# Kernel optimization log

Hardware: AMD Instinct MI355X
Metric: run time of the kernel (lower is better)

Reference implementation:

```python
import jax, jax.numpy as jnp
import numpy as np

M_POOL = 5000  # rows of down_transform (coarse mesh size)


def setup_inputs() -> dict:
    key = jax.random.key(0)
    ks = jax.random.split(key, 6)
    bs, n_nodes, c_in, seq_len, c_out = 16, 20000, 32, 9, 64
    x = jax.random.normal(ks[0], (bs, n_nodes, c_in), dtype=jnp.float32)
    indices = jax.random.randint(ks[1], (n_nodes, seq_len), 0, n_nodes, dtype=jnp.int32)
    # xavier-uniform-ish linear weight
    fan_in, fan_out = c_in * seq_len, c_out
    limit = float(np.sqrt(6.0 / (fan_in + fan_out)))
    weight = jax.random.uniform(ks[2], (c_out, fan_in), minval=-limit, maxval=limit, dtype=jnp.float32)
    bias = jnp.zeros((c_out,), dtype=jnp.float32)
    trans_rows = jax.random.randint(ks[3], (20000,), 0, M_POOL, dtype=jnp.int32)
    trans_cols = jax.random.randint(ks[4], (20000,), 0, n_nodes, dtype=jnp.int32)
    trans_vals = jax.random.uniform(ks[5], (20000,), dtype=jnp.float32)
    return {"x": x, "indices": indices, "weight": weight, "bias": bias,
            "trans_rows": trans_rows, "trans_cols": trans_cols, "trans_vals": trans_vals}


def reference(x, indices, weight, bias, trans_rows, trans_cols, trans_vals):
    bs = x.shape[0]
    n_nodes, seq_len = indices.shape
    # SpiralConv: gather spiral neighborhoods -> [bs, n_nodes, seq_len*c_in]
    g = x[:, indices.reshape(-1), :].reshape(bs, n_nodes, -1)
    h = jnp.einsum('bnk,ok->bno', g, weight) + bias  # [bs, n_nodes, c_out]
    h = jax.nn.elu(h)
    # Pool: sparse down_transform @ h  (scatter_add over COO entries)
    contrib = h[:, trans_cols, :] * trans_vals[None, :, None]  # [bs, nnz, c_out]
    out = jnp.zeros((bs, M_POOL, h.shape[-1]), dtype=h.dtype)
    out = out.at[:, trans_rows, :].add(contrib)
    return out
```

## Files before the change

kernel.cpp:

```cpp
#include <hip/hip_runtime.h>

#define BS 16
#define NNODES 20000
#define CIN 32
#define SEQ 9
#define COUT 64
#define KTOT 288
#define MPOOL 5000
#define NNZ 20000

#define H_BYTES   40960000ULL
#define XB_BYTES  20480000ULL
#define WF_BYTES  36864ULL
#define CV_BYTES  (NNZ * 8ULL)
#define START_BYTES ((MPOOL + 1) * 4ULL)
#define CNTCUR_BYTES (2ULL * MPOOL * 4ULL)

#define XBLK (NNODES / 4)
#define WBLK 9
#define ZBLK 10

typedef __attribute__((ext_vector_type(8))) short bf16x8;
typedef __attribute__((ext_vector_type(4))) float f32x4;

static __device__ __forceinline__ unsigned short f2bf(float f) {
  unsigned u = __float_as_uint(f);
  u += 0x7FFF + ((u >> 16) & 1);
  return (unsigned short)(u >> 16);
}
static __device__ __forceinline__ float bf2f(unsigned short s) {
  return __uint_as_float(((unsigned)s) << 16);
}
static __device__ __forceinline__ unsigned cvt_pk_bf16(float lo, float hi) {
  unsigned r;
  asm("v_cvt_pk_bf16_f32 %0, %1, %2" : "=v"(r) : "v"(lo), "v"(hi));
  return r;
}

__global__ __launch_bounds__(256) void prep_kernel(const float* __restrict__ x,
                                                   const float* __restrict__ weight,
                                                   unsigned short* __restrict__ xbT2,
                                                   unsigned short* __restrict__ wf,
                                                   int* __restrict__ cntcur) {
  const int id = blockIdx.x;
  if (id < XBLK) {
    const int W = id * 4 + (threadIdx.x >> 6);
    const int lane = threadIdx.x & 63;
    const unsigned b = (unsigned)W / 1250u;
    const unsigned tile = (unsigned)W % 1250u;
    const int n = (int)tile * 16 + (lane >> 2);
    const int c8 = (lane & 3) * 8;
    const float* src = x + ((size_t)b * NNODES + n) * CIN + c8;
    const float4 u0 = ((const float4*)src)[0];
    const float4 u1 = ((const float4*)src)[1];
    uint4 p;
    p.x = (unsigned)f2bf(u0.x) | ((unsigned)f2bf(u0.y) << 16);
    p.y = (unsigned)f2bf(u0.z) | ((unsigned)f2bf(u0.w) << 16);
    p.z = (unsigned)f2bf(u1.x) | ((unsigned)f2bf(u1.y) << 16);
    p.w = (unsigned)f2bf(u1.z) | ((unsigned)f2bf(u1.w) << 16);
    const int g = (int)(b >> 1), bl = (int)(b & 1);
    *(uint4*)&xbT2[((size_t)g * NNODES + n) * 64 + bl * 32 + c8] = p;
  } else if (id < XBLK + WBLK) {
    const int t = (id - XBLK) * 256 + threadIdx.x;
    if (t < SEQ * 4 * 64) {
      const int f0 = t * 8;
      const int blk = f0 >> 9;
      const int inb = f0 & 511;
      const int lhi = inb >> 7;
      const int l16 = (inb >> 3) & 15;
      const int kk = blk >> 2, o = blk & 3;
      const float* src = weight + (size_t)(o * 16 + l16) * KTOT + kk * 32 + lhi * 8;
      const float4 u0 = ((const float4*)src)[0];
      const float4 u1 = ((const float4*)src)[1];
      uint4 p;
      p.x = (unsigned)f2bf(u0.x) | ((unsigned)f2bf(u0.y) << 16);
      p.y = (unsigned)f2bf(u0.z) | ((unsigned)f2bf(u0.w) << 16);
      p.z = (unsigned)f2bf(u1.x) | ((unsigned)f2bf(u1.y) << 16);
      p.w = (unsigned)f2bf(u1.z) | ((unsigned)f2bf(u1.w) << 16);
      *(uint4*)&wf[f0] = p;
    }
  } else {
    const int base = (id - XBLK - WBLK) * 1024 + threadIdx.x;
#pragma unroll
    for (int j = 0; j < 4; ++j) {
      const int i = base + j * 256;
      if (i < 2 * MPOOL) cntcur[i] = 0;
    }
  }
}

__global__ __launch_bounds__(256) void hist_kernel(const int* __restrict__ rows,
                                                   int* __restrict__ cnt) {
  const int k = blockIdx.x * 256 + threadIdx.x;
  if (k < NNZ) atomicAdd(&cnt[rows[k]], 1);
}

__global__ __launch_bounds__(256) void scan_kernel(const int* __restrict__ cnt,
                                                   int* __restrict__ start) {
  __shared__ int part[256];
  const int t = threadIdx.x;
  const int base = t * 20;
  int local[20];
  int s = 0;
#pragma unroll
  for (int j = 0; j < 20; ++j) {
    const int i = base + j;
    local[j] = s;
    s += (i < MPOOL) ? cnt[i] : 0;
  }
  part[t] = s;
  __syncthreads();
  for (int off = 1; off < 256; off <<= 1) {
    const int v = (t >= off) ? part[t - off] : 0;
    __syncthreads();
    part[t] += v;
    __syncthreads();
  }
  const int excl = (t == 0) ? 0 : part[t - 1];
#pragma unroll
  for (int j = 0; j < 20; ++j) {
    const int i = base + j;
    if (i < MPOOL) start[i] = excl + local[j];
  }
  if (t == 255) start[MPOOL] = NNZ;
}

__global__ __launch_bounds__(256) void reorder_kernel(const int* __restrict__ rows,
                                                      const int* __restrict__ cols,
                                                      const float* __restrict__ vals,
                                                      const int* __restrict__ start,
                                                      int* __restrict__ cursor,
                                                      int2* __restrict__ cvp) {
  const int k = blockIdx.x * 256 + threadIdx.x;
  if (k < NNZ) {
    const int r = rows[k];
    const int pos = start[r] + atomicAdd(&cursor[r], 1);
    cvp[pos] = make_int2(cols[k], __float_as_int(vals[k]));
  }
}

__global__ __launch_bounds__(512, 8) void gemm_elu_kernel(
    const unsigned short* __restrict__ xbT2,
    const int* __restrict__ indices,
    const unsigned short* __restrict__ wf,
    const float* __restrict__ bias,
    unsigned* __restrict__ hT)
{
  __shared__ unsigned short wlds[SEQ * 4 * 512];
  __shared__ int idx_lds[64 * SEQ];

  const int tid = threadIdx.x;
  const int g = blockIdx.x & 7;
  const int n0 = (blockIdx.x >> 3) * 64;

  {
    const uint4* src = (const uint4*)wf;
    uint4* dst = (uint4*)wlds;
    for (int i = tid; i < (SEQ * 4 * 512 * 2) / 16; i += 512)
      dst[i] = src[i];
  }
  for (int i = tid; i < 64 * SEQ; i += 512) {
    const int gidx = n0 * SEQ + i;
    idx_lds[i] = (gidx < NNODES * SEQ) ? indices[gidx] : 0;
  }
  __syncthreads();

  const int wv = tid >> 6;
  const int lane = tid & 63;
  const int l16 = lane & 15;
  const int lhi = lane >> 4;
  const int n0w = n0 + wv * 8;
  if (n0w >= NNODES) return;

  const unsigned short* __restrict__ xg = xbT2 + (size_t)g * NNODES * 64;
  const int moff = (l16 & 1) * 32 + lhi * 8;
  const int boff = lane * 8;
  const int idxbase = (wv * 8 + (l16 >> 1)) * SEQ;

  f32x4 acc[4];
#pragma unroll
  for (int o = 0; o < 4; ++o) {
    f32x4 z = {0.f, 0.f, 0.f, 0.f};
    acc[o] = z;
  }

#pragma unroll
  for (int kk = 0; kk < SEQ; ++kk) {
    const int gi = idx_lds[idxbase + kk];
    const bf16x8 af = *(const bf16x8*)&xg[(size_t)gi * 64 + moff];
    const bf16x8 b0 = *(const bf16x8*)&wlds[(kk * 4 + 0) * 512 + boff];
    const bf16x8 b1 = *(const bf16x8*)&wlds[(kk * 4 + 1) * 512 + boff];
    const bf16x8 b2 = *(const bf16x8*)&wlds[(kk * 4 + 2) * 512 + boff];
    const bf16x8 b3 = *(const bf16x8*)&wlds[(kk * 4 + 3) * 512 + boff];
    acc[0] = __builtin_amdgcn_mfma_f32_16x16x32_bf16(af, b0, acc[0], 0, 0, 0);
    acc[1] = __builtin_amdgcn_mfma_f32_16x16x32_bf16(af, b1, acc[1], 0, 0, 0);
    acc[2] = __builtin_amdgcn_mfma_f32_16x16x32_bf16(af, b2, acc[2], 0, 0, 0);
    acc[3] = __builtin_amdgcn_mfma_f32_16x16x32_bf16(af, b3, acc[3], 0, 0, 0);
  }

  unsigned* __restrict__ hg = hT + (size_t)g * NNODES * 64;
  const int nA = n0w + lhi * 2;
#pragma unroll
  for (int o = 0; o < 4; ++o) {
    const int oc = o * 16 + l16;
    const float bv = bias[oc];
    float v0 = acc[o][0] + bv, v1 = acc[o][1] + bv;
    float v2 = acc[o][2] + bv, v3 = acc[o][3] + bv;
    v0 = v0 > 0.f ? v0 : (__expf(v0) - 1.f);
    v1 = v1 > 0.f ? v1 : (__expf(v1) - 1.f);
    v2 = v2 > 0.f ? v2 : (__expf(v2) - 1.f);
    v3 = v3 > 0.f ? v3 : (__expf(v3) - 1.f);
    hg[(size_t)nA * 64 + oc]       = cvt_pk_bf16(v0, v1);
    hg[(size_t)(nA + 1) * 64 + oc] = cvt_pk_bf16(v2, v3);
  }
}

__global__ __launch_bounds__(256) void pool_kernel(
    const unsigned* __restrict__ hT,
    const int* __restrict__ start,
    const int2* __restrict__ cvp,
    float* __restrict__ out)
{
  const int r = blockIdx.x * 4 + (threadIdx.x >> 6);
  const int lane = threadIdx.x & 63;

  float acc[16];
#pragma unroll
  for (int b = 0; b < 16; ++b) acc[b] = 0.f;

  const int s = start[r], e = start[r + 1];
  int2 cv = (s < e) ? cvp[s] : make_int2(0, 0);
  for (int j = s; j < e; ++j) {
    const int2 cvn = (j + 1 < e) ? cvp[j + 1] : make_int2(0, 0);
    const int c = cv.x;
    const float v = __int_as_float(cv.y);
#pragma unroll
    for (int g = 0; g < 8; ++g) {
      const unsigned u = hT[((size_t)g * NNODES + c) * 64 + lane];
      acc[2 * g]     += v * bf2f((unsigned short)(u & 0xffff));
      acc[2 * g + 1] += v * bf2f((unsigned short)(u >> 16));
    }
    cv = cvn;
  }
#pragma unroll
  for (int b = 0; b < 16; ++b)
    out[((size_t)b * MPOOL + r) * COUT + lane] = acc[b];
}

__global__ __launch_bounds__(256) void scatter_kernel(
    const unsigned* __restrict__ hT,
    const int* __restrict__ rows,
    const int* __restrict__ cols,
    const float* __restrict__ vals,
    float* __restrict__ out)
{
  const int gw = (int)((blockIdx.x * blockDim.x + threadIdx.x) >> 6);
  const int lane = threadIdx.x & 63;
  const int nw = (int)((gridDim.x * blockDim.x) >> 6);
  for (int t = gw; t < NNZ * BS; t += nw) {
    const int k = t >> 4;
    const int b = t & 15;
    const unsigned u = hT[((size_t)(b >> 1) * NNODES + cols[k]) * 64 + lane];
    const float hv = bf2f((unsigned short)((b & 1) ? (u >> 16) : (u & 0xffff)));
    atomicAdd(&out[((size_t)b * MPOOL + rows[k]) * COUT + lane], hv * vals[k]);
  }
}

extern "C" void kernel_launch(void* const* d_in, const int* in_sizes, int n_in,
                              void* d_out, int out_size, void* d_ws, size_t ws_size,
                              hipStream_t stream) {
  const float* x       = (const float*)d_in[0];
  const int*   indices = (const int*)d_in[1];
  const float* weight  = (const float*)d_in[2];
  const float* bias    = (const float*)d_in[3];
  const int*   trows   = (const int*)d_in[4];
  const int*   tcols   = (const int*)d_in[5];
  const float* tvals   = (const float*)d_in[6];
  float* out = (float*)d_out;

  char* w = (char*)d_ws;
  unsigned* hT         = (unsigned*)w;
  unsigned short* xbT2 = (unsigned short*)(w + H_BYTES);
  unsigned short* wf   = (unsigned short*)(w + H_BYTES + XB_BYTES);
  int2* cvp  = (int2*)(w + H_BYTES + XB_BYTES + WF_BYTES);
  int* start = (int*)(w + H_BYTES + XB_BYTES + WF_BYTES + CV_BYTES);
  int* cnt   = (int*)(w + H_BYTES + XB_BYTES + WF_BYTES + CV_BYTES + START_BYTES);
  int* cursor = cnt + MPOOL;

  const bool big_ws = (ws_size >=
      H_BYTES + XB_BYTES + WF_BYTES + CV_BYTES + START_BYTES + CNTCUR_BYTES);

  prep_kernel<<<XBLK + WBLK + ZBLK, 256, 0, stream>>>(x, weight, xbT2, wf, cnt);

  if (big_ws) {
    hist_kernel<<<(NNZ + 255) / 256, 256, 0, stream>>>(trows, cnt);
    scan_kernel<<<1, 256, 0, stream>>>(cnt, start);
    reorder_kernel<<<(NNZ + 255) / 256, 256, 0, stream>>>(trows, tcols, tvals,
                                                          start, cursor, cvp);
  }

  gemm_elu_kernel<<<313 * 8, 512, 0, stream>>>(xbT2, indices, wf, bias, hT);

  if (big_ws) {
    pool_kernel<<<MPOOL / 4, 256, 0, stream>>>(hT, start, cvp, out);
  } else {
    hipMemsetAsync(d_out, 0, (size_t)out_size * sizeof(float), stream);
    scatter_kernel<<<4096, 256, 0, stream>>>(hT, trows, tcols, tvals, out);
  }
}
```

Measured before the change: 61.49 us.

## Fold CSR build into extra GEMM block using LDS histogram and scan

```diff
diff --git a/kernel.cpp b/kernel.cpp
--- a/kernel.cpp
+++ b/kernel.cpp
@@ -14,11 +14,10 @@
 #define WF_BYTES  36864ULL
 #define CV_BYTES  (NNZ * 8ULL)
 #define START_BYTES ((MPOOL + 1) * 4ULL)
-#define CNTCUR_BYTES (2ULL * MPOOL * 4ULL)
 
 #define XBLK (NNODES / 4)
 #define WBLK 9
-#define ZBLK 10
+#define NTILE8 (313 * 8)
 
 typedef __attribute__((ext_vector_type(8))) short bf16x8;
 typedef __attribute__((ext_vector_type(4))) float f32x4;
@@ -40,8 +39,7 @@
 __global__ __launch_bounds__(256) void prep_kernel(const float* __restrict__ x,
                                                    const float* __restrict__ weight,
                                                    unsigned short* __restrict__ xbT2,
-                                                   unsigned short* __restrict__ wf,
-                                                   int* __restrict__ cntcur) {
+                                                   unsigned short* __restrict__ wf) {
   const int id = blockIdx.x;
   if (id < XBLK) {
     const int W = id * 4 + (threadIdx.x >> 6);
@@ -60,7 +58,7 @@
     p.w = (unsigned)f2bf(u1.z) | ((unsigned)f2bf(u1.w) << 16);
     const int g = (int)(b >> 1), bl = (int)(b & 1);
     *(uint4*)&xbT2[((size_t)g * NNODES + n) * 64 + bl * 32 + c8] = p;
-  } else if (id < XBLK + WBLK) {
+  } else {
     const int t = (id - XBLK) * 256 + threadIdx.x;
     if (t < SEQ * 4 * 64) {
       const int f0 = t * 8;
@@ -79,77 +77,70 @@
       p.w = (unsigned)f2bf(u1.z) | ((unsigned)f2bf(u1.w) << 16);
       *(uint4*)&wf[f0] = p;
     }
-  } else {
-    const int base = (id - XBLK - WBLK) * 1024 + threadIdx.x;
-#pragma unroll
-    for (int j = 0; j < 4; ++j) {
-      const int i = base + j * 256;
-      if (i < 2 * MPOOL) cntcur[i] = 0;
-    }
-  }
-}
-
-__global__ __launch_bounds__(256) void hist_kernel(const int* __restrict__ rows,
-                                                   int* __restrict__ cnt) {
-  const int k = blockIdx.x * 256 + threadIdx.x;
-  if (k < NNZ) atomicAdd(&cnt[rows[k]], 1);
-}
-
-__global__ __launch_bounds__(256) void scan_kernel(const int* __restrict__ cnt,
-                                                   int* __restrict__ start) {
-  __shared__ int part[256];
-  const int t = threadIdx.x;
-  const int base = t * 20;
-  int local[20];
-  int s = 0;
-#pragma unroll
-  for (int j = 0; j < 20; ++j) {
-    const int i = base + j;
-    local[j] = s;
-    s += (i < MPOOL) ? cnt[i] : 0;
-  }
-  part[t] = s;
-  __syncthreads();
-  for (int off = 1; off < 256; off <<= 1) {
-    const int v = (t >= off) ? part[t - off] : 0;
-    __syncthreads();
-    part[t] += v;
-    __syncthreads();
-  }
-  const int excl = (t == 0) ? 0 : part[t - 1];
-#pragma unroll
-  for (int j = 0; j < 20; ++j) {
-    const int i = base + j;
-    if (i < MPOOL) start[i] = excl + local[j];
-  }
-  if (t == 255) start[MPOOL] = NNZ;
-}
-
-__global__ __launch_bounds__(256) void reorder_kernel(const int* __restrict__ rows,
-                                                      const int* __restrict__ cols,
-                                                      const float* __restrict__ vals,
-                                                      const int* __restrict__ start,
-                                                      int* __restrict__ cursor,
-                                                      int2* __restrict__ cvp) {
-  const int k = blockIdx.x * 256 + threadIdx.x;
-  if (k < NNZ) {
-    const int r = rows[k];
-    const int pos = start[r] + atomicAdd(&cursor[r], 1);
-    cvp[pos] = make_int2(cols[k], __float_as_int(vals[k]));
-  }
-}
-
-__global__ __launch_bounds__(512, 8) void gemm_elu_kernel(
+  }
+}
+
+__global__ __launch_bounds__(512, 4) void gemm_elu_kernel(
     const unsigned short* __restrict__ xbT2,
     const int* __restrict__ indices,
     const unsigned short* __restrict__ wf,
     const float* __restrict__ bias,
-    unsigned* __restrict__ hT)
+    unsigned* __restrict__ hT,
+    const int* __restrict__ trows,
+    const int* __restrict__ tcols,
+    const float* __restrict__ tvals,
+    int* __restrict__ start,
+    int2* __restrict__ cvp)
 {
   __shared__ unsigned short wlds[SEQ * 4 * 512];
   __shared__ int idx_lds[64 * SEQ];
 
   const int tid = threadIdx.x;
+
+  if (blockIdx.x == NTILE8) {
+    int* lcnt = (int*)wlds;
+    int* part = (int*)idx_lds;
+    for (int i = tid; i < MPOOL; i += 512) lcnt[i] = 0;
+    __syncthreads();
+    for (int k = tid; k < NNZ; k += 512) atomicAdd(&lcnt[trows[k]], 1);
+    __syncthreads();
+    int local[10];
+    int s = 0;
+    const int base = tid * 10;
+#pragma unroll
+    for (int j = 0; j < 10; ++j) {
+      const int i = base + j;
+      local[j] = s;
+      s += (i < MPOOL) ? lcnt[i] : 0;
+    }
+    part[tid] = s;
+    __syncthreads();
+    for (int off = 1; off < 512; off <<= 1) {
+      const int v = (tid >= off) ? part[tid - off] : 0;
+      __syncthreads();
+      part[tid] += v;
+      __syncthreads();
+    }
+    const int excl = (tid == 0) ? 0 : part[tid - 1];
+    __syncthreads();
+#pragma unroll
+    for (int j = 0; j < 10; ++j) {
+      const int i = base + j;
+      if (i < MPOOL) {
+        const int sv = excl + local[j];
+        start[i] = sv;
+        lcnt[i] = sv;
+      }
+    }
+    if (tid == 0) start[MPOOL] = NNZ;
+    __syncthreads();
+    for (int k = tid; k < NNZ; k += 512) {
+      const int pos = atomicAdd(&lcnt[trows[k]], 1);
+      cvp[pos] = make_int2(tcols[k], __float_as_int(tvals[k]));
+    }
+    return;
+  }
+
   const int g = blockIdx.x & 7;
   const int n0 = (blockIdx.x >> 3) * 64;
 
@@ -284,22 +275,14 @@
   unsigned short* wf   = (unsigned short*)(w + H_BYTES + XB_BYTES);
   int2* cvp  = (int2*)(w + H_BYTES + XB_BYTES + WF_BYTES);
   int* start = (int*)(w + H_BYTES + XB_BYTES + WF_BYTES + CV_BYTES);
-  int* cnt   = (int*)(w + H_BYTES + XB_BYTES + WF_BYTES + CV_BYTES + START_BYTES);
-  int* cursor = cnt + MPOOL;
-
-  const bool big_ws = (ws_size >=
-      H_BYTES + XB_BYTES + WF_BYTES + CV_BYTES + START_BYTES + CNTCUR_BYTES);
-
-  prep_kernel<<<XBLK + WBLK + ZBLK, 256, 0, stream>>>(x, weight, xbT2, wf, cnt);
-
-  if (big_ws) {
-    hist_kernel<<<(NNZ + 255) / 256, 256, 0, stream>>>(trows, cnt);
-    scan_kernel<<<1, 256, 0, stream>>>(cnt, start);
-    reorder_kernel<<<(NNZ + 255) / 256, 256, 0, stream>>>(trows, tcols, tvals,
-                                                          start, cursor, cvp);
-  }
-
-  gemm_elu_kernel<<<313 * 8, 512, 0, stream>>>(xbT2, indices, wf, bias, hT);
+
+  const bool big_ws =
+      (ws_size >= H_BYTES + XB_BYTES + WF_BYTES + CV_BYTES + START_BYTES);
+
+  prep_kernel<<<XBLK + WBLK, 256, 0, stream>>>(x, weight, xbT2, wf);
+
+  gemm_elu_kernel<<<big_ws ? (NTILE8 + 1) : NTILE8, 512, 0, stream>>>(
+      xbT2, indices, wf, bias, hT, trows, tcols, tvals, start, cvp);
 
   if (big_ws) {
     pool_kernel<<<MPOOL / 4, 256, 0, stream>>>(hT, start, cvp, out);
```

New measurement: 82.31 us. 33.9% more time.
